# Optimization experiments

Measured on AMD Instinct MI355X. Metric: run time of the kernel, lower is better.

## Reference

```python
import jax, jax.numpy as jnp
import numpy as np

B, N, D, H, C, TOPK = 1, 1024, 1024, 16, 64, 2
HD = D // H   # head_dim = 64
G = N // C    # num blocks = 16


def setup_inputs() -> dict:
    key = jax.random.key(0)
    ks = jax.random.split(key, 6)
    s = 0.02  # init_std
    x = jax.random.normal(ks[0], (B, N, D), jnp.float32)
    Wq = jax.random.normal(ks[1], (D, D), jnp.float32) * s
    Wk = jax.random.normal(ks[2], (D, D), jnp.float32) * s
    Wv = jax.random.normal(ks[3], (D, D), jnp.float32) * s
    Wg = jax.random.normal(ks[4], (2 * H, D), jnp.float32) * s
    Wo = jax.random.normal(ks[5], (D, D), jnp.float32) * s
    return {"x": x, "Wq": Wq, "Wk": Wk, "Wv": Wv, "Wg": Wg, "Wo": Wo}


def reference(x, Wq, Wk, Wv, Wg, Wo):
    b, n, d = x.shape
    h, c, hd, g = H, C, HD, G
    scale = hd ** -0.5
    # projections (torch Linear: x @ W.T)
    q = (x @ Wq.T).reshape(b, n, h, hd)
    k = (x @ Wk.T).reshape(b, n, h, hd)
    v = (x @ Wv.T).reshape(b, n, h, hd)
    gate = jax.nn.softmax((x @ Wg.T).reshape(b, n, h, 2), axis=-1)
    # chunked views: (b, g, c, h, hd)
    kc = k.reshape(b, g, c, h, hd)
    vc = v.reshape(b, g, c, h, hd)
    # compressed block keys: mean over chunk dim -> (b, g, h, hd)
    k_compress = kc.mean(axis=2)
    # block selection scores (b, h, n, g)
    score = jnp.einsum('bnhd,bghd->bhng', q, k_compress)
    pos = jnp.arange(n)[:, None]
    blk = jnp.arange(g)[None, :]
    mask = pos >= c * blk  # (n, g), exactly as source's _get_mask (masked_fill where True)
    score = jnp.where(mask[None, None], -jnp.inf, score)
    idx = jax.lax.top_k(score, TOPK)[1]  # (b, h, n, top_k), int indices
    # gather selected blocks per (batch, head, query)
    k_bhgcd = kc.transpose(0, 3, 1, 2, 4)  # (b, h, g, c, hd)
    v_bhgcd = vc.transpose(0, 3, 1, 2, 4)
    gather = jax.vmap(jax.vmap(lambda kv, i: kv[i]))  # over b, h
    k_sel = gather(k_bhgcd, idx).reshape(b, h, n, TOPK * c, hd)
    v_sel = gather(v_bhgcd, idx).reshape(b, h, n, TOPK * c, hd)
    # inter: per-query attention over gathered KV (non-causal), flash-attn scale 1/sqrt(hd)
    logits = jnp.einsum('bnhd,bhnld->bhnl', q, k_sel) * scale
    p = jax.nn.softmax(logits, axis=-1)
    o_inter = jnp.einsum('bhnl,bhnld->bnhd', p, v_sel)
    # intra: causal attention within each chunk
    qc = q.reshape(b, g, c, h, hd)
    intra = jnp.einsum('bgihd,bgjhd->bghij', qc, kc) * scale
    cm = jnp.tril(jnp.ones((c, c), dtype=bool))
    intra = jnp.where(cm, intra, -jnp.inf)
    pi = jax.nn.softmax(intra, axis=-1)
    o_intra = jnp.einsum('bghij,bgjhd->bgihd', pi, vc).reshape(b, n, h, hd)
    # gated blend + output projection
    o = gate[..., 0:1] * o_inter + gate[..., 1:2] * o_intra  # (b, n, h, hd)
    return o.reshape(b, n, h * hd) @ Wo.T
```

## Files before the change

kernel.cpp:

```cpp
#include <hip/hip_runtime.h>
#include <hip/hip_bf16.h>
#include <math.h>


typedef __attribute__((ext_vector_type(8))) short short8;
typedef __attribute__((ext_vector_type(4))) float f32x4;

#define NTOK 1024
#define DMODEL 1024
#define NHEAD 16
#define HDIM 64
#define CHUNK 64
#define NBLK 16

__device__ __forceinline__ float qmax16(float v)
{
    #pragma unroll
    for (int off = 1; off < 16; off <<= 1) v = fmaxf(v, __shfl_xor(v, off));
    return v;
}

__device__ __forceinline__ float qsum16(float v)
{
    #pragma unroll
    for (int off = 1; off < 16; off <<= 1) v += __shfl_xor(v, off);
    return v;
}


#define GLOAD_LDS16(gp, lp)                                              \
    __builtin_amdgcn_global_load_lds(                                    \
        (const __attribute__((address_space(1))) void*)(gp),             \
        (__attribute__((address_space(3))) void*)(lp), 16, 0, 0)

__device__ __forceinline__ void stage64(const __hip_bfloat16* __restrict__ g0,
                                        __hip_bfloat16* t, int wave, int lane)
{
    const int sub = lane >> 3;
    const int cch = (lane & 7) ^ sub;
    #pragma unroll
    for (int j = 0; j < 2; j++) {
        const int rr = (2 * wave + j) * 8 + sub;
        GLOAD_LDS16(g0 + (size_t)rr * DMODEL + cch * 8, t + (2 * wave + j) * 512);
    }
}

__device__ __forceinline__ void stage64w8(const __hip_bfloat16* __restrict__ g0,
                                          __hip_bfloat16* t, int wave, int lane)
{
    const int sub = lane >> 3;
    const int cch = (lane & 7) ^ sub;
    GLOAD_LDS16(g0 + (size_t)(wave * 8 + sub) * DMODEL + cch * 8, t + wave * 512);
}

__device__ __forceinline__ short8 ldsfrag(const __hip_bfloat16* t, int row, int chunk)
{
    return *(const short8*)((const char*)t + row * 128 + (((chunk) ^ (row & 7)) << 4));
}

__global__ __launch_bounds__(256) void prep_kernel(
    const float* __restrict__ x,  const float* __restrict__ Wq,
    const float* __restrict__ Wk, const float* __restrict__ Wv,
    const float* __restrict__ Wo, const float* __restrict__ Wg,
    __hip_bfloat16* __restrict__ xh,  __hip_bfloat16* __restrict__ xl,
    __hip_bfloat16* __restrict__ Wqh,
    __hip_bfloat16* __restrict__ Wkh, __hip_bfloat16* __restrict__ Wvh,
    __hip_bfloat16* __restrict__ Woh, __hip_bfloat16* __restrict__ Wol,
    float* __restrict__ xm, float2* __restrict__ gate)
{
    __shared__ float gs[32];
    const int bid = blockIdx.x;
    if (bid < 5120) {
        const int which = bid >> 10;
        const int b = bid & 1023;
        const int i = (b * 256 + threadIdx.x) * 4;
        const float* in; __hip_bfloat16 *hi, *lo = nullptr;
        if (which == 0)      { in = x;  hi = xh;  lo = xl; }
        else if (which == 1) { in = Wq; hi = Wqh; }
        else if (which == 2) { in = Wk; hi = Wkh; }
        else if (which == 3) { in = Wv; hi = Wvh; }
        else                 { in = Wo; hi = Woh; lo = Wol; }
        float4 v = *(const float4*)(in + i);
        float vv[4] = {v.x, v.y, v.z, v.w};
        __hip_bfloat16 h[4], l[4];
        #pragma unroll
        for (int j = 0; j < 4; j++) {
            h[j] = __float2bfloat16(vv[j]);
            l[j] = __float2bfloat16(vv[j] - __bfloat162float(h[j]));
        }
        *(uint2*)(hi + i) = *(uint2*)h;
        if (lo) *(uint2*)(lo + i) = *(uint2*)l;
    } else if (bid < 5184) {
        const int b = bid - 5120;
        const int g = b >> 2;
        const int f = (b & 3) * 256 + threadIdx.x;
        float s = 0.f;
        #pragma unroll 8
        for (int c = 0; c < CHUNK; c++) s += x[(size_t)(g * CHUNK + c) * DMODEL + f];
        xm[g * DMODEL + f] = s * (1.0f / CHUNK);
    } else {
        const int n = bid - 5184;
        const int wave = threadIdx.x >> 6, lane = threadIdx.x & 63;
        #pragma unroll
        for (int jj = 0; jj < 8; jj++) {
            int j = wave * 8 + jj;
            float s = 0.f;
            #pragma unroll
            for (int t = 0; t < 16; t++) {
                int d = lane + (t << 6);
                s += x[n * DMODEL + d] * Wg[j * DMODEL + d];
            }
            #pragma unroll
            for (int off = 32; off; off >>= 1) s += __shfl_xor(s, off);
            if (lane == 0) gs[j] = s;
        }
        __syncthreads();
        if (threadIdx.x < NHEAD) {
            int h = threadIdx.x;
            float a = gs[2 * h], b = gs[2 * h + 1];
            float m = fmaxf(a, b);
            float ea = expf(a - m), eb = expf(b - m);
            float inv = 1.f / (ea + eb);
            gate[n * NHEAD + h] = make_float2(ea * inv, eb * inv);
        }
    }
}

__global__ __launch_bounds__(256) void kc_gemm_kernel(
    const float* __restrict__ xm, const float* __restrict__ Wk,
    float* __restrict__ kc)
{
    const int f = blockIdx.x;
    const int g = threadIdx.x >> 4;
    const int sub = threadIdx.x & 15;
    const float* wrow = Wk + (size_t)f * DMODEL;
    float s = 0.f;
    #pragma unroll 16
    for (int i = 0; i < 64; i++) {
        int e = i * 16 + sub;
        s += xm[g * DMODEL + e] * wrow[e];
    }
    #pragma unroll
    for (int off = 8; off; off >>= 1) s += __shfl_xor(s, off);
    if (sub == 0) kc[g * DMODEL + f] = s;
}

__global__ __launch_bounds__(256) void u_kernel(
    const float* __restrict__ kc, const float* __restrict__ Wq,
    __hip_bfloat16* __restrict__ Uh, __hip_bfloat16* __restrict__ Ul)
{
    __shared__ float kcs[64];
    const int h = blockIdx.x >> 4, g = blockIdx.x & 15;
    if (threadIdx.x < 64) kcs[threadIdx.x] = kc[g * DMODEL + h * HDIM + threadIdx.x];
    __syncthreads();
    const int col = (h << 4) | g;
    for (int f = threadIdx.x; f < DMODEL; f += 256) {
        float s = 0.f;
        #pragma unroll 16
        for (int d = 0; d < 64; d++)
            s += kcs[d] * Wq[(size_t)(h * HDIM + d) * DMODEL + f];
        __hip_bfloat16 hv = __float2bfloat16(s);
        Uh[(size_t)col * DMODEL + f] = hv;
        Ul[(size_t)col * DMODEL + f] = __float2bfloat16(s - __bfloat162float(hv));
    }
}

__global__ __launch_bounds__(256) void qkv_score_kernel(
    const __hip_bfloat16* __restrict__ xh, const __hip_bfloat16* __restrict__ xl,
    const __hip_bfloat16* __restrict__ Wqh, const __hip_bfloat16* __restrict__ Wkh,
    const __hip_bfloat16* __restrict__ Wvh,
    const __hip_bfloat16* __restrict__ Uh, const __hip_bfloat16* __restrict__ Ul,
    __hip_bfloat16* __restrict__ Qb, __hip_bfloat16* __restrict__ Kb,
    __hip_bfloat16* __restrict__ Vt, float* __restrict__ S)
{
    __shared__ alignas(16) char smem[32768];
    __hip_bfloat16* AshP = (__hip_bfloat16*)smem;
    __hip_bfloat16* AslP = (__hip_bfloat16*)(smem + 8192);
    __hip_bfloat16* BshP = (__hip_bfloat16*)(smem + 16384);
    __hip_bfloat16* BslP = (__hip_bfloat16*)(smem + 24576);

    const int b = blockIdx.x;
    const int tid  = threadIdx.x;
    const int wave = tid >> 6;
    const int lane = tid & 63;
    const int lr = tid >> 2;
    const int lc = (tid & 3) * 16;
    const int wm = (wave >> 1) * 32;
    const int wn = (wave & 1) * 32;
    const int fr = lane & 15;
    const int quad = lane >> 4;

    if (b < 768) {
        const int widx = b >> 8;
        const int t = b & 255;
        const __hip_bfloat16* __restrict__ Bh =
            (widx == 0) ? Wqh : (widx == 1) ? Wkh : Wvh;
        const int n0 = (t & 15) * 64;
        const int m0 = (t >> 4) * 64;

        f32x4 acc[2][2] = {};

        for (int k0 = 0; k0 < DMODEL; k0 += 64) {
            stage64(xh + (size_t)m0 * DMODEL + k0, AshP, wave, lane);
            stage64(Bh + (size_t)n0 * DMODEL + k0, BshP, wave, lane);
            __syncthreads();

            #pragma unroll
            for (int hk = 0; hk < 2; hk++) {
                const int ch = hk * 4 + quad;
                short8 a0 = ldsfrag(AshP, wm + fr, ch);
                short8 a1 = ldsfrag(AshP, wm + 16 + fr, ch);
                short8 b0 = ldsfrag(BshP, wn + fr, ch);
                short8 b1 = ldsfrag(BshP, wn + 16 + fr, ch);
                acc[0][0] = __builtin_amdgcn_mfma_f32_16x16x32_bf16(a0, b0, acc[0][0], 0, 0, 0);
                acc[0][1] = __builtin_amdgcn_mfma_f32_16x16x32_bf16(a0, b1, acc[0][1], 0, 0, 0);
                acc[1][0] = __builtin_amdgcn_mfma_f32_16x16x32_bf16(a1, b0, acc[1][0], 0, 0, 0);
                acc[1][1] = __builtin_amdgcn_mfma_f32_16x16x32_bf16(a1, b1, acc[1][1], 0, 0, 0);
            }
            __syncthreads();
        }

        if (widx == 0) {
            #pragma unroll
            for (int tm = 0; tm < 2; tm++)
            #pragma unroll
            for (int tn = 0; tn < 2; tn++)
            #pragma unroll
            for (int r = 0; r < 4; r++) {
                int row = m0 + wm + tm * 16 + quad * 4 + r;
                int col = n0 + wn + tn * 16 + fr;
                Qb[(size_t)row * DMODEL + col] = __float2bfloat16(acc[tm][tn][r]);
            }
        } else if (widx == 1) {
            #pragma unroll
            for (int tm = 0; tm < 2; tm++)
            #pragma unroll
            for (int tn = 0; tn < 2; tn++)
            #pragma unroll
            for (int r = 0; r < 4; r++) {
                int row = m0 + wm + tm * 16 + quad * 4 + r;
                int col = n0 + wn + tn * 16 + fr;
                Kb[(size_t)row * DMODEL + col] = __float2bfloat16(acc[tm][tn][r]);
            }
        } else {
            __hip_bfloat16 (*T)[72] = (__hip_bfloat16(*)[72])smem;
            #pragma unroll
            for (int tm = 0; tm < 2; tm++)
            #pragma unroll
            for (int tn = 0; tn < 2; tn++)
            #pragma unroll
            for (int r = 0; r < 4; r++) {
                int nloc = wm + tm * 16 + quad * 4 + r;
                int floc = wn + tn * 16 + fr;
                T[floc][nloc] = __float2bfloat16(acc[tm][tn][r]);
            }
            __syncthreads();
            const size_t o = (size_t)(n0 + lr) * NTOK + m0 + lc;
            *(uint4*)(Vt + o)     = *(uint4*)(&T[lr][lc]);
            *(uint4*)(Vt + o + 8) = *(uint4*)(&T[lr][lc + 8]);
        }
    } else {
        const int bb = b - 768;
        const int m0 = (bb >> 2) * 64;
        const int n0 = (bb & 3) * 64;

        f32x4 acc[2][2] = {};

        for (int k0 = 0; k0 < DMODEL; k0 += 64) {
            stage64(xh + (size_t)m0 * DMODEL + k0, AshP, wave, lane);
            stage64(xl + (size_t)m0 * DMODEL + k0, AslP, wave, lane);
            stage64(Uh + (size_t)n0 * DMODEL + k0, BshP, wave, lane);
            stage64(Ul + (size_t)n0 * DMODEL + k0, BslP, wave, lane);
            __syncthreads();

            #pragma unroll
            for (int hk = 0; hk < 2; hk++) {
                const int ch = hk * 4 + quad;
                short8 a0h = ldsfrag(AshP, wm + fr, ch);
                short8 a1h = ldsfrag(AshP, wm + 16 + fr, ch);
                short8 a0l = ldsfrag(AslP, wm + fr, ch);
                short8 a1l = ldsfrag(AslP, wm + 16 + fr, ch);
                short8 b0h = ldsfrag(BshP, wn + fr, ch);
                short8 b1h = ldsfrag(BshP, wn + 16 + fr, ch);
                short8 b0l = ldsfrag(BslP, wn + fr, ch);
                short8 b1l = ldsfrag(BslP, wn + 16 + fr, ch);
                acc[0][0] = __builtin_amdgcn_mfma_f32_16x16x32_bf16(a0l, b0h, acc[0][0], 0, 0, 0);
                acc[0][1] = __builtin_amdgcn_mfma_f32_16x16x32_bf16(a0l, b1h, acc[0][1], 0, 0, 0);
                acc[1][0] = __builtin_amdgcn_mfma_f32_16x16x32_bf16(a1l, b0h, acc[1][0], 0, 0, 0);
                acc[1][1] = __builtin_amdgcn_mfma_f32_16x16x32_bf16(a1l, b1h, acc[1][1], 0, 0, 0);
                acc[0][0] = __builtin_amdgcn_mfma_f32_16x16x32_bf16(a0h, b0l, acc[0][0], 0, 0, 0);
                acc[0][1] = __builtin_amdgcn_mfma_f32_16x16x32_bf16(a0h, b1l, acc[0][1], 0, 0, 0);
                acc[1][0] = __builtin_amdgcn_mfma_f32_16x16x32_bf16(a1h, b0l, acc[1][0], 0, 0, 0);
                acc[1][1] = __builtin_amdgcn_mfma_f32_16x16x32_bf16(a1h, b1l, acc[1][1], 0, 0, 0);
                acc[0][0] = __builtin_amdgcn_mfma_f32_16x16x32_bf16(a0h, b0h, acc[0][0], 0, 0, 0);
                acc[0][1] = __builtin_amdgcn_mfma_f32_16x16x32_bf16(a0h, b1h, acc[0][1], 0, 0, 0);
                acc[1][0] = __builtin_amdgcn_mfma_f32_16x16x32_bf16(a1h, b0h, acc[1][0], 0, 0, 0);
                acc[1][1] = __builtin_amdgcn_mfma_f32_16x16x32_bf16(a1h, b1h, acc[1][1], 0, 0, 0);
            }
            __syncthreads();
        }

        #pragma unroll
        for (int tm = 0; tm < 2; tm++)
        #pragma unroll
        for (int tn = 0; tn < 2; tn++)
        #pragma unroll
        for (int r = 0; r < 4; r++) {
            int row = m0 + wm + tm * 16 + quad * 4 + r;
            int col = n0 + wn + tn * 16 + fr;
            S[(size_t)row * 256 + col] = acc[tm][tn][r];
        }
    }
}

__global__ __launch_bounds__(256, 4) void attn_mfma_kernel(
    const __hip_bfloat16* __restrict__ Qb, const __hip_bfloat16* __restrict__ Kb,
    const __hip_bfloat16* __restrict__ Vt, const float* __restrict__ S,
    const float2* __restrict__ gate, __hip_bfloat16* __restrict__ oh)
{
    __shared__ float OS[4][16][64];
    __shared__ float OIs[16][64];
    __shared__ float mS[4][16], lS[4][16], liS[16];
    __shared__ int i1s[16], i2s[16];
    __shared__ float2 sgate[16];
    __shared__ unsigned unionMask;
    __shared__ __hip_bfloat16 Ps[4][16][72];

    const int bid = blockIdx.x;
    const int qt = bid & 3;
    const int h  = (bid >> 2) & 15;
    const int g  = bid >> 6;
    const int tid = threadIdx.x;
    const int s = tid >> 6;
    const int lane = tid & 63;
    const int fr = lane & 15, quad = lane >> 4;

    if (tid < 16) {
        const int n = g * 64 + qt * 16 + tid;
        const float* Sn = S + (size_t)n * 256 + h * 16;
        float sc[NBLK];
        #pragma unroll
        for (int gg = 0; gg < NBLK; gg++)
            sc[gg] = (n >= (gg << 6)) ? -INFINITY : Sn[gg];
        int i1 = -1, i2 = -1;
        float b1 = -INFINITY;
        #pragma unroll
        for (int gg = 0; gg < NBLK; gg++) if (i1 < 0 || sc[gg] > b1) { b1 = sc[gg]; i1 = gg; }
        float b2 = -INFINITY;
        #pragma unroll
        for (int gg = 0; gg < NBLK; gg++) { if (gg == i1) continue; if (i2 < 0 || sc[gg] > b2) { b2 = sc[gg]; i2 = gg; } }
        i1s[tid] = i1; i2s[tid] = i2;
        sgate[tid] = gate[(size_t)n * NHEAD + h];
        unsigned m = (1u << i1) | (1u << i2);
        #pragma unroll
        for (int off = 1; off < 16; off <<= 1) m |= (unsigned)__shfl_xor((int)m, off);
        if (tid == 0) unionMask = m;
    }
    __syncthreads();

    const unsigned um = unionMask;

    const size_t qrow = (size_t)(g * 64 + qt * 16 + fr) * DMODEL + h * HDIM + quad * 8;
    const short8 qa0 = *(const short8*)(Qb + qrow);
    const short8 qa1 = *(const short8*)(Qb + qrow + 32);

    int qi1[4], qi2[4];
    #pragma unroll
    for (int r = 0; r < 4; r++) {
        int q = quad * 4 + r;
        qi1[r] = i1s[q]; qi2[r] = i2s[q];
    }

    f32x4 Oint[4] = {};
    float mrun[4] = {-INFINITY, -INFINITY, -INFINITY, -INFINITY};
    float lrun[4] = {0.f, 0.f, 0.f, 0.f};

    const __hip_bfloat16* __restrict__ Kh = Kb + h * HDIM + quad * 8;
    const __hip_bfloat16* __restrict__ Vh = Vt + (size_t)(h * HDIM) * NTOK + quad * 8;

    int j = 0;
    for (int kb = 0; kb < NBLK; kb++) {
        if (!((um >> kb) & 1u)) continue;
        if ((j++ & 3) != s) continue;

        f32x4 sacc[4] = {};
        #pragma unroll
        for (int t = 0; t < 4; t++) {
            const size_t krow = (size_t)(kb * 64 + t * 16 + fr) * DMODEL;
            short8 kb0 = *(const short8*)(Kh + krow);
            short8 kb1 = *(const short8*)(Kh + krow + 32);
            sacc[t] = __builtin_amdgcn_mfma_f32_16x16x32_bf16(qa0, kb0, sacc[t], 0, 0, 0);
            sacc[t] = __builtin_amdgcn_mfma_f32_16x16x32_bf16(qa1, kb1, sacc[t], 0, 0, 0);
        }

        #pragma unroll
        for (int r = 0; r < 4; r++) {
            const bool sel = (kb == qi1[r]) | (kb == qi2[r]);
            float v0 = sacc[0][r] * 0.125f, v1 = sacc[1][r] * 0.125f;
            float v2 = sacc[2][r] * 0.125f, v3 = sacc[3][r] * 0.125f;
            float mx = qmax16(fmaxf(fmaxf(v0, v1), fmaxf(v2, v3)));
            float mnew = sel ? fmaxf(mrun[r], mx) : mrun[r];
            float f = sel ? __expf(mrun[r] - mnew) : 1.0f;
            float e0 = sel ? __expf(v0 - mnew) : 0.f;
            float e1 = sel ? __expf(v1 - mnew) : 0.f;
            float e2 = sel ? __expf(v2 - mnew) : 0.f;
            float e3 = sel ? __expf(v3 - mnew) : 0.f;
            float es = qsum16(e0 + e1 + e2 + e3);
            lrun[r] = lrun[r] * f + es;
            mrun[r] = mnew;
            #pragma unroll
            for (int dn = 0; dn < 4; dn++) Oint[dn][r] *= f;
            const int prow = quad * 4 + r;
            Ps[s][prow][ 0 + fr] = __float2bfloat16(e0);
            Ps[s][prow][16 + fr] = __float2bfloat16(e1);
            Ps[s][prow][32 + fr] = __float2bfloat16(e2);
            Ps[s][prow][48 + fr] = __float2bfloat16(e3);
        }

        short8 pa0 = *(const short8*)(&Ps[s][fr][quad * 8]);
        short8 pa1 = *(const short8*)(&Ps[s][fr][32 + quad * 8]);
        #pragma unroll
        for (int dn = 0; dn < 4; dn++) {
            const size_t vrow = (size_t)(dn * 16 + fr) * NTOK + kb * 64;
            short8 v0 = *(const short8*)(Vh + vrow);
            short8 v1 = *(const short8*)(Vh + vrow + 32);
            Oint[dn] = __builtin_amdgcn_mfma_f32_16x16x32_bf16(pa0, v0, Oint[dn], 0, 0, 0);
            Oint[dn] = __builtin_amdgcn_mfma_f32_16x16x32_bf16(pa1, v1, Oint[dn], 0, 0, 0);
        }
    }

    if ((j & 3) == s) {
        f32x4 sacc[4] = {};
        #pragma unroll
        for (int t = 0; t < 4; t++) {
            const size_t krow = (size_t)(g * 64 + t * 16 + fr) * DMODEL;
            short8 kb0 = *(const short8*)(Kh + krow);
            short8 kb1 = *(const short8*)(Kh + krow + 32);
            sacc[t] = __builtin_amdgcn_mfma_f32_16x16x32_bf16(qa0, kb0, sacc[t], 0, 0, 0);
            sacc[t] = __builtin_amdgcn_mfma_f32_16x16x32_bf16(qa1, kb1, sacc[t], 0, 0, 0);
        }
        f32x4 Ointr[4] = {};
        #pragma unroll
        for (int r = 0; r < 4; r++) {
            const int qloc = qt * 16 + quad * 4 + r;
            float vv[4];
            #pragma unroll
            for (int t = 0; t < 4; t++) {
                const int col = t * 16 + fr;
                float v = sacc[t][r] * 0.125f;
                vv[t] = (col <= qloc) ? v : -INFINITY;
            }
            float mx = qmax16(fmaxf(fmaxf(vv[0], vv[1]), fmaxf(vv[2], vv[3])));
            float e0 = __expf(vv[0] - mx), e1 = __expf(vv[1] - mx);
            float e2 = __expf(vv[2] - mx), e3 = __expf(vv[3] - mx);
            float lsum = qsum16(e0 + e1 + e2 + e3);
            const int prow = quad * 4 + r;
            if (fr == 0) liS[prow] = lsum;
            Ps[s][prow][ 0 + fr] = __float2bfloat16(e0);
            Ps[s][prow][16 + fr] = __float2bfloat16(e1);
            Ps[s][prow][32 + fr] = __float2bfloat16(e2);
            Ps[s][prow][48 + fr] = __float2bfloat16(e3);
        }
        short8 pa0 = *(const short8*)(&Ps[s][fr][quad * 8]);
        short8 pa1 = *(const short8*)(&Ps[s][fr][32 + quad * 8]);
        f32x4 Ointr2[4] = {};
        #pragma unroll
        for (int dn = 0; dn < 4; dn++) {
            const size_t vrow = (size_t)(dn * 16 + fr) * NTOK + g * 64;
            short8 v0 = *(const short8*)(Vh + vrow);
            short8 v1 = *(const short8*)(Vh + vrow + 32);
            Ointr2[dn] = __builtin_amdgcn_mfma_f32_16x16x32_bf16(pa0, v0, Ointr[dn], 0, 0, 0);
            Ointr2[dn] = __builtin_amdgcn_mfma_f32_16x16x32_bf16(pa1, v1, Ointr2[dn], 0, 0, 0);
        }
        #pragma unroll
        for (int r = 0; r < 4; r++)
        #pragma unroll
        for (int dn = 0; dn < 4; dn++)
            OIs[quad * 4 + r][dn * 16 + fr] = Ointr2[dn][r];
    }

    #pragma unroll
    for (int r = 0; r < 4; r++) {
        if (fr == 0) { mS[s][quad * 4 + r] = mrun[r]; lS[s][quad * 4 + r] = lrun[r]; }
        #pragma unroll
        for (int dn = 0; dn < 4; dn++)
            OS[s][quad * 4 + r][dn * 16 + fr] = Oint[dn][r];
    }
    __syncthreads();

    {
        const int q = tid >> 4;
        const int db = (tid & 15) * 4;
        float M = fmaxf(fmaxf(mS[0][q], mS[1][q]), fmaxf(mS[2][q], mS[3][q]));
        float L = 0.f;
        float o0 = 0.f, o1 = 0.f, o2 = 0.f, o3 = 0.f;
        #pragma unroll
        for (int ss = 0; ss < 4; ss++) {
            float p = __expf(mS[ss][q] - M);
            L += lS[ss][q] * p;
            o0 += OS[ss][q][db + 0] * p;
            o1 += OS[ss][q][db + 1] * p;
            o2 += OS[ss][q][db + 2] * p;
            o3 += OS[ss][q][db + 3] * p;
        }
        const float2 gt = sgate[q];
        const float wi = gt.x / L;
        const float wl = gt.y / liS[q];
        unsigned short out4[4];
        out4[0] = __builtin_bit_cast(unsigned short, __float2bfloat16(wi * o0 + wl * OIs[q][db + 0]));
        out4[1] = __builtin_bit_cast(unsigned short, __float2bfloat16(wi * o1 + wl * OIs[q][db + 1]));
        out4[2] = __builtin_bit_cast(unsigned short, __float2bfloat16(wi * o2 + wl * OIs[q][db + 2]));
        out4[3] = __builtin_bit_cast(unsigned short, __float2bfloat16(wi * o3 + wl * OIs[q][db + 3]));
        const int n = g * 64 + qt * 16 + q;
        *(uint2*)(oh + (size_t)n * DMODEL + h * HDIM + db) = *(uint2*)out4;
    }
}

__global__ __launch_bounds__(512) void gemm_wo(
    const __hip_bfloat16* __restrict__ Ah,
    const __hip_bfloat16* __restrict__ Bh, const __hip_bfloat16* __restrict__ Bl,
    float* __restrict__ C)
{
    __shared__ alignas(16) char smem[24576];
    __hip_bfloat16* AshP = (__hip_bfloat16*)smem;
    __hip_bfloat16* BshP = (__hip_bfloat16*)(smem + 8192);
    __hip_bfloat16* BslP = (__hip_bfloat16*)(smem + 16384);

    const int n0 = blockIdx.x * 64;
    const int m0 = blockIdx.y * 64;

    const int tid  = threadIdx.x;
    const int wave = tid >> 6;
    const int lane = tid & 63;
    const int wm = (wave >> 1) * 16;
    const int wn = (wave & 1) * 32;
    const int fr = lane & 15;
    const int quad = lane >> 4;

    f32x4 acc[2] = {};

    for (int k0 = 0; k0 < DMODEL; k0 += 64) {
        stage64w8(Ah + (size_t)m0 * DMODEL + k0, AshP, wave, lane);
        stage64w8(Bh + (size_t)n0 * DMODEL + k0, BshP, wave, lane);
        stage64w8(Bl + (size_t)n0 * DMODEL + k0, BslP, wave, lane);
        __syncthreads();

        #pragma unroll
        for (int hk = 0; hk < 2; hk++) {
            const int ch = hk * 4 + quad;
            short8 a0  = ldsfrag(AshP, wm + fr, ch);
            short8 b0h = ldsfrag(BshP, wn + fr, ch);
            short8 b1h = ldsfrag(BshP, wn + 16 + fr, ch);
            short8 b0l = ldsfrag(BslP, wn + fr, ch);
            short8 b1l = ldsfrag(BslP, wn + 16 + fr, ch);
            acc[0] = __builtin_amdgcn_mfma_f32_16x16x32_bf16(a0, b0l, acc[0], 0, 0, 0);
            acc[1] = __builtin_amdgcn_mfma_f32_16x16x32_bf16(a0, b1l, acc[1], 0, 0, 0);
            acc[0] = __builtin_amdgcn_mfma_f32_16x16x32_bf16(a0, b0h, acc[0], 0, 0, 0);
            acc[1] = __builtin_amdgcn_mfma_f32_16x16x32_bf16(a0, b1h, acc[1], 0, 0, 0);
        }
        __syncthreads();
    }

    #pragma unroll
    for (int tn = 0; tn < 2; tn++)
    #pragma unroll
    for (int r = 0; r < 4; r++) {
        int row = m0 + wm + quad * 4 + r;
        int col = n0 + wn + tn * 16 + fr;
        C[(size_t)row * DMODEL + col] = acc[tn][r];
    }
}

extern "C" void kernel_launch(void* const* d_in, const int* in_sizes, int n_in,
                              void* d_out, int out_size, void* d_ws, size_t ws_size,
                              hipStream_t stream)
{
    const float* x  = (const float*)d_in[0];
    const float* Wq = (const float*)d_in[1];
    const float* Wk = (const float*)d_in[2];
    const float* Wv = (const float*)d_in[3];
    const float* Wg = (const float*)d_in[4];
    const float* Wo = (const float*)d_in[5];

    const size_t M1 = (size_t)NTOK * DMODEL;

    float* S       = (float*)d_ws;
    float* xm      = S + (size_t)NTOK * 256;
    float* kc      = xm + NBLK * DMODEL;
    float2* gate   = (float2*)(kc + NBLK * DMODEL);
    __hip_bfloat16* xh  = (__hip_bfloat16*)(gate + NTOK * NHEAD);
    __hip_bfloat16* xl  = xh + M1;
    __hip_bfloat16* Wqh = xl + M1;
    __hip_bfloat16* Wkh = Wqh + M1;
    __hip_bfloat16* Wvh = Wkh + M1;
    __hip_bfloat16* Woh = Wvh + M1;
    __hip_bfloat16* Wol = Woh + M1;
    __hip_bfloat16* oh  = Wol + M1;
    __hip_bfloat16* Uh  = oh + M1;
    __hip_bfloat16* Ul  = Uh + 256 * DMODEL;
    __hip_bfloat16* Qb  = Ul + 256 * DMODEL;
    __hip_bfloat16* Kb  = Qb + M1;
    __hip_bfloat16* Vt  = Kb + M1;

    prep_kernel<<<6208, 256, 0, stream>>>(
        x, Wq, Wk, Wv, Wo, Wg, xh, xl, Wqh, Wkh, Wvh, Woh, Wol, xm, gate);

    kc_gemm_kernel<<<1024, 256, 0, stream>>>(xm, Wk, kc);
    u_kernel<<<256, 256, 0, stream>>>(kc, Wq, Uh, Ul);

    qkv_score_kernel<<<832, 256, 0, stream>>>(
        xh, xl, Wqh, Wkh, Wvh, Uh, Ul, Qb, Kb, Vt, S);

    attn_mfma_kernel<<<NBLK * NHEAD * 4, 256, 0, stream>>>(Qb, Kb, Vt, S, gate, oh);

    dim3 gwo(16, 16);
    gemm_wo<<<gwo, 512, 0, stream>>>(oh, Woh, Wol, (float*)d_out);
}
```

Measured before the change: 161.8 us.

## Use 128x128 double-buffered tiles for QKV projection GEMM

The Q/K/V projection part of qkv_score_kernel moves from 64x64 tiles (768 blocks) to 128x128 tiles (192 blocks). Each wave now computes a 64x64 sub-tile with a 4x4 MFMA accumulator grid. LDS is doubled to 64KB and used as a double buffer, so the next K-slice is prefetched while the current one is consumed, with one barrier per iteration. This aims to raise arithmetic intensity and hide load latency. The cost is fewer blocks (256 total, close to the CU count), higher register pressure, and lower occupancy from the 64KB LDS footprint. The V-transpose epilogue is split into two passes to fit the shared staging buffer.

```diff
diff --git a/kernel.cpp b/kernel.cpp
--- a/kernel.cpp
+++ b/kernel.cpp
@@ -42,6 +42,18 @@
     for (int j = 0; j < 2; j++) {
         const int rr = (2 * wave + j) * 8 + sub;
         GLOAD_LDS16(g0 + (size_t)rr * DMODEL + cch * 8, t + (2 * wave + j) * 512);
+    }
+}
+
+__device__ __forceinline__ void stage128(const __hip_bfloat16* __restrict__ g0,
+                                         __hip_bfloat16* t, int wave, int lane)
+{
+    const int sub = lane >> 3;
+    const int cch = (lane & 7) ^ sub;
+    #pragma unroll
+    for (int j = 0; j < 4; j++) {
+        const int grp = wave * 4 + j;
+        GLOAD_LDS16(g0 + (size_t)(grp * 8 + sub) * DMODEL + cch * 8, t + grp * 512);
     }
 }
 
@@ -173,94 +185,111 @@
     __hip_bfloat16* __restrict__ Qb, __hip_bfloat16* __restrict__ Kb,
     __hip_bfloat16* __restrict__ Vt, float* __restrict__ S)
 {
-    __shared__ alignas(16) char smem[32768];
-    __hip_bfloat16* AshP = (__hip_bfloat16*)smem;
-    __hip_bfloat16* AslP = (__hip_bfloat16*)(smem + 8192);
-    __hip_bfloat16* BshP = (__hip_bfloat16*)(smem + 16384);
-    __hip_bfloat16* BslP = (__hip_bfloat16*)(smem + 24576);
+    __shared__ alignas(16) char smem[65536];
 
     const int b = blockIdx.x;
     const int tid  = threadIdx.x;
     const int wave = tid >> 6;
     const int lane = tid & 63;
-    const int lr = tid >> 2;
-    const int lc = (tid & 3) * 16;
-    const int wm = (wave >> 1) * 32;
-    const int wn = (wave & 1) * 32;
     const int fr = lane & 15;
     const int quad = lane >> 4;
 
-    if (b < 768) {
-        const int widx = b >> 8;
-        const int t = b & 255;
-        const __hip_bfloat16* __restrict__ Bh =
+    if (b < 192) {
+        __hip_bfloat16* A0 = (__hip_bfloat16*)smem;
+        __hip_bfloat16* B0 = (__hip_bfloat16*)(smem + 16384);
+        __hip_bfloat16* A1 = (__hip_bfloat16*)(smem + 32768);
+        __hip_bfloat16* B1 = (__hip_bfloat16*)(smem + 49152);
+
+        const int widx = b >> 6;
+        const int t = b & 63;
+        const int m0 = (t >> 3) * 128;
+        const int n0 = (t & 7) * 128;
+        const __hip_bfloat16* __restrict__ Bw =
             (widx == 0) ? Wqh : (widx == 1) ? Wkh : Wvh;
-        const int n0 = (t & 15) * 64;
-        const int m0 = (t >> 4) * 64;
-
-        f32x4 acc[2][2] = {};
-
-        for (int k0 = 0; k0 < DMODEL; k0 += 64) {
-            stage64(xh + (size_t)m0 * DMODEL + k0, AshP, wave, lane);
-            stage64(Bh + (size_t)n0 * DMODEL + k0, BshP, wave, lane);
-            __syncthreads();
-
+
+        const int wm = (wave >> 1) * 64;
+        const int wn = (wave & 1) * 64;
+
+        f32x4 acc[4][4] = {};
+
+        stage128(xh + (size_t)m0 * DMODEL, A0, wave, lane);
+        stage128(Bw + (size_t)n0 * DMODEL, B0, wave, lane);
+        __syncthreads();
+
+        for (int kt = 0; kt < 16; kt++) {
+            const int cur = kt & 1;
+            __hip_bfloat16* Ac = cur ? A1 : A0;
+            __hip_bfloat16* Bc = cur ? B1 : B0;
+            if (kt < 15) {
+                __hip_bfloat16* An = cur ? A0 : A1;
+                __hip_bfloat16* Bn = cur ? B0 : B1;
+                stage128(xh + (size_t)m0 * DMODEL + (kt + 1) * 64, An, wave, lane);
+                stage128(Bw + (size_t)n0 * DMODEL + (kt + 1) * 64, Bn, wave, lane);
+            }
             #pragma unroll
             for (int hk = 0; hk < 2; hk++) {
                 const int ch = hk * 4 + quad;
-                short8 a0 = ldsfrag(AshP, wm + fr, ch);
-                short8 a1 = ldsfrag(AshP, wm + 16 + fr, ch);
-                short8 b0 = ldsfrag(BshP, wn + fr, ch);
-                short8 b1 = ldsfrag(BshP, wn + 16 + fr, ch);
-                acc[0][0] = __builtin_amdgcn_mfma_f32_16x16x32_bf16(a0, b0, acc[0][0], 0, 0, 0);
-                acc[0][1] = __builtin_amdgcn_mfma_f32_16x16x32_bf16(a0, b1, acc[0][1], 0, 0, 0);
-                acc[1][0] = __builtin_amdgcn_mfma_f32_16x16x32_bf16(a1, b0, acc[1][0], 0, 0, 0);
-                acc[1][1] = __builtin_amdgcn_mfma_f32_16x16x32_bf16(a1, b1, acc[1][1], 0, 0, 0);
+                short8 am[4], bn[4];
+                #pragma unroll
+                for (int i = 0; i < 4; i++) am[i] = ldsfrag(Ac, wm + i * 16 + fr, ch);
+                #pragma unroll
+                for (int j = 0; j < 4; j++) bn[j] = ldsfrag(Bc, wn + j * 16 + fr, ch);
+                #pragma unroll
+                for (int i = 0; i < 4; i++)
+                #pragma unroll
+                for (int j = 0; j < 4; j++)
+                    acc[i][j] = __builtin_amdgcn_mfma_f32_16x16x32_bf16(am[i], bn[j], acc[i][j], 0, 0, 0);
             }
             __syncthreads();
         }
 
-        if (widx == 0) {
-            #pragma unroll
-            for (int tm = 0; tm < 2; tm++)
-            #pragma unroll
-            for (int tn = 0; tn < 2; tn++)
+        if (widx == 0 || widx == 1) {
+            __hip_bfloat16* __restrict__ Out = (widx == 0) ? Qb : Kb;
+            #pragma unroll
+            for (int i = 0; i < 4; i++)
+            #pragma unroll
+            for (int j = 0; j < 4; j++)
             #pragma unroll
             for (int r = 0; r < 4; r++) {
-                int row = m0 + wm + tm * 16 + quad * 4 + r;
-                int col = n0 + wn + tn * 16 + fr;
-                Qb[(size_t)row * DMODEL + col] = __float2bfloat16(acc[tm][tn][r]);
-            }
-        } else if (widx == 1) {
-            #pragma unroll
-            for (int tm = 0; tm < 2; tm++)
-            #pragma unroll
-            for (int tn = 0; tn < 2; tn++)
-            #pragma unroll
-            for (int r = 0; r < 4; r++) {
-                int row = m0 + wm + tm * 16 + quad * 4 + r;
-                int col = n0 + wn + tn * 16 + fr;
-                Kb[(size_t)row * DMODEL + col] = __float2bfloat16(acc[tm][tn][r]);
+                int row = m0 + wm + i * 16 + quad * 4 + r;
+                int col = n0 + wn + j * 16 + fr;
+                Out[(size_t)row * DMODEL + col] = __float2bfloat16(acc[i][j][r]);
             }
         } else {
-            __hip_bfloat16 (*T)[72] = (__hip_bfloat16(*)[72])smem;
-            #pragma unroll
-            for (int tm = 0; tm < 2; tm++)
-            #pragma unroll
-            for (int tn = 0; tn < 2; tn++)
-            #pragma unroll
-            for (int r = 0; r < 4; r++) {
-                int nloc = wm + tm * 16 + quad * 4 + r;
-                int floc = wn + tn * 16 + fr;
-                T[floc][nloc] = __float2bfloat16(acc[tm][tn][r]);
+            __hip_bfloat16 (*T)[136] = (__hip_bfloat16(*)[136])smem;
+            for (int p = 0; p < 2; p++) {
+                __syncthreads();
+                if ((wn >> 6) == p) {
+                    #pragma unroll
+                    for (int i = 0; i < 4; i++)
+                    #pragma unroll
+                    for (int j = 0; j < 4; j++)
+                    #pragma unroll
+                    for (int r = 0; r < 4; r++) {
+                        int nloc = wm + i * 16 + quad * 4 + r;
+                        int floc = (wn - p * 64) + j * 16 + fr;
+                        T[floc][nloc] = __float2bfloat16(acc[i][j][r]);
+                    }
+                }
+                __syncthreads();
+                const int row = tid >> 2;
+                const int cb  = (tid & 3) * 32;
+                const size_t o = (size_t)(n0 + p * 64 + row) * NTOK + m0 + cb;
+                #pragma unroll
+                for (int u = 0; u < 4; u++)
+                    *(uint4*)(Vt + o + u * 8) = *(uint4*)(&T[row][cb + u * 8]);
             }
-            __syncthreads();
-            const size_t o = (size_t)(n0 + lr) * NTOK + m0 + lc;
-            *(uint4*)(Vt + o)     = *(uint4*)(&T[lr][lc]);
-            *(uint4*)(Vt + o + 8) = *(uint4*)(&T[lr][lc + 8]);
         }
     } else {
-        const int bb = b - 768;
+        __hip_bfloat16* AshP = (__hip_bfloat16*)smem;
+        __hip_bfloat16* AslP = (__hip_bfloat16*)(smem + 8192);
+        __hip_bfloat16* BshP = (__hip_bfloat16*)(smem + 16384);
+        __hip_bfloat16* BslP = (__hip_bfloat16*)(smem + 24576);
+
+        const int wm = (wave >> 1) * 32;
+        const int wn = (wave & 1) * 32;
+
+        const int bb = b - 192;
         const int m0 = (bb >> 2) * 64;
         const int n0 = (bb & 3) * 64;
 
@@ -608,7 +637,7 @@
     kc_gemm_kernel<<<1024, 256, 0, stream>>>(xm, Wk, kc);
     u_kernel<<<256, 256, 0, stream>>>(kc, Wq, Uh, Ul);
 
-    qkv_score_kernel<<<832, 256, 0, stream>>>(
+    qkv_score_kernel<<<256, 256, 0, stream>>>(
         xh, xl, Wqh, Wkh, Wvh, Uh, Ul, Qb, Kb, Vt, S);
 
     attn_mfma_kernel<<<NBLK * NHEAD * 4, 256, 0, stream>>>(Qb, Kb, Vt, S, gate, oh);
```

Measured after the change: 158.9 us. Within noise of the previous version (-1.8%).
